# Kernel tuning notes

Measured on AMD Instinct MI355X. Metric: run time of the kernel, lower is better.

## Reference

```python
import jax, jax.numpy as jnp
import numpy as np

B, S, D, H, IT, V = 2, 1024, 1024, 8, 28, 50257
DH = D // H
EPS = jnp.float32(1.1920929e-07)  # torch RMSNorm default eps = finfo(float32).eps


def _rmsnorm(x, w):
    # torch nn.RMSNorm: x * rsqrt(mean(x^2) + eps) * weight
    ms = jnp.mean(jnp.square(x), axis=-1, keepdims=True)
    return x * jax.lax.rsqrt(ms + EPS) * w


def setup_inputs() -> dict:
    key = jax.random.key(0)
    ks = jax.random.split(key, 8)
    s = 0.02
    tokens = jax.random.randint(ks[0], (B, S), 0, V)
    embed = jax.random.normal(ks[1], (V, D), dtype=jnp.float32) * s
    Wk = jax.random.normal(ks[2], (D, D), dtype=jnp.float32) * s
    Wv = jax.random.normal(ks[3], (D, D), dtype=jnp.float32) * s
    Ws = jax.random.normal(ks[4], (D, D), dtype=jnp.float32) * s
    Wo = jax.random.normal(ks[5], (D, D), dtype=jnp.float32) * s  # original zero-inits; randomized for a non-trivial baseline
    step_size = jnp.linspace(0.5, 0.1, IT, dtype=jnp.float32)
    norm_w = jnp.ones((IT, D), jnp.float32)   # per-iteration RMSNorm weight
    gamma = jnp.ones((IT, D), jnp.float32)
    beta = jnp.zeros((IT, D), jnp.float32)
    out_norm_w = jnp.ones((D,), jnp.float32)
    lm_head_w = jax.random.normal(ks[6], (V, D), dtype=jnp.float32) * s
    return dict(tokens=tokens, embed=embed, Wk=Wk, Wv=Wv, Ws=Ws, Wo=Wo,
                step_size=step_size, norm_w=norm_w, gamma=gamma, beta=beta,
                out_norm_w=out_norm_w, lm_head_w=lm_head_w)


def _forward(tokens, embed, Wk, Wv, Ws, Wo, step_size, norm_w, gamma, beta, out_norm_w, lm_head_w):
    b, s = tokens.shape
    causal = jnp.tril(jnp.ones((s, s), dtype=bool))  # allow j <= i
    scale = 1.0 / np.sqrt(DH)

    def compute_force(h):
        k = (h @ Wk.T).reshape(b, s, H, DH)
        v = (h @ Wv.T).reshape(b, s, H, DH)
        energy = jnp.einsum('bihd,bjhd->bhij', k, k) * scale
        logits = jnp.where(causal, -energy, -jnp.inf)  # softmax(-energy) with causal masking
        w = jax.nn.softmax(logits, axis=-1)
        pairwise = jnp.einsum('bhij,bjhd->bihd', w, v).reshape(b, s, D)
        return (pairwise + h @ Ws.T) @ Wo.T

    def step(x, p):
        st, nw, g, bb = p
        h = _rmsnorm(x, nw) * g + bb
        return x + compute_force(h) * st, None

    x0 = embed[tokens].astype(jnp.float32)
    x, _ = jax.lax.scan(jax.checkpoint(step), x0, (step_size, norm_w, gamma, beta))
    x = _rmsnorm(x, out_norm_w)
    return x @ lm_head_w.T  # [B, S, V] logits


def reference(tokens, embed, Wk, Wv, Ws, Wo, step_size, norm_w, gamma, beta, out_norm_w, lm_head_w):
    return _forward(tokens, embed, Wk, Wv, Ws, Wo, step_size, norm_w, gamma, beta, out_norm_w, lm_head_w)
```

## Files before the change

kernel.cpp:

```cpp
#include <hip/hip_runtime.h>
#include <cstdint>
#include <cstddef>

#define S_   1024
#define D_   1024
#define H_   8
#define DH_  128
#define IT_  28
#define V_   50257
#define B_   2
#define ROWS 2048
#define EPS_ 1.1920929e-07f

typedef unsigned short u16;
typedef __attribute__((ext_vector_type(8))) short s8v;
typedef __attribute__((ext_vector_type(4))) float f4v;

static __device__ __forceinline__ void gload16(const void* g, void* l) {
  __builtin_amdgcn_global_load_lds((__attribute__((address_space(1))) void*)(g),
                                   (__attribute__((address_space(3))) void*)(l), 16, 0, 0);
}

static __device__ __forceinline__ u16 f2bf(float f) {
  union { float f; uint32_t u; } v; v.f = f;
  return (u16)((v.u + 0x7FFFu + ((v.u >> 16) & 1u)) >> 16);
}

static __device__ __forceinline__ float wave_sum(float v) {
#pragma unroll
  for (int o = 32; o > 0; o >>= 1) v += __shfl_xor(v, o, 64);
  return v;
}

__device__ __constant__ int IT_TAB[40] = {
  15,15,15,15, 14,14,14, 13,13,13, 12,12,12, 11,11,11,
  10,10, 9,9, 8,8, 7,7, 6, 5, 4, 3,
  14,10,6,2, 13,9,5,1, 12,8,4,0};
__device__ __constant__ int CH_TAB[40] = {
  0,1,2,3, 0,1,2, 0,1,2, 0,1,2, 0,1,2,
  0,1, 0,1, 0,1, 0,1, 0, 0, 0, 0,
  3,2,1,0, 3,2,1,0, 3,2,1,0};

__global__ __launch_bounds__(256) void k_embed(const int* __restrict__ tok,
                                               const float* __restrict__ emb,
                                               float* __restrict__ x) {
  const int row = blockIdx.x;
  const int t = tok[row];
  ((float4*)(x + (size_t)row * D_))[threadIdx.x] =
      ((const float4*)(emb + (size_t)t * D_))[threadIdx.x];
}

__global__ __launch_bounds__(256) void k_cvt(const float* __restrict__ w,
                                             u16* __restrict__ o, int n4) {
  const int idx = blockIdx.x * 256 + threadIdx.x;
  if (idx < n4) {
    const float4 f = ((const float4*)w)[idx];
    ushort4 u;
    u.x = f2bf(f.x); u.y = f2bf(f.y); u.z = f2bf(f.z); u.w = f2bf(f.w);
    ((ushort4*)o)[idx] = u;
  }
}

__global__ __launch_bounds__(256) void k_rmsnorm(const float* __restrict__ x,
                                                 const float* __restrict__ nw,
                                                 const float* __restrict__ g,
                                                 const float* __restrict__ bb,
                                                 u16* __restrict__ h) {
  const int row = blockIdx.x;
  const int tid = threadIdx.x;
  const float4 xv = ((const float4*)(x + (size_t)row * D_))[tid];
  float ss = xv.x*xv.x + xv.y*xv.y + xv.z*xv.z + xv.w*xv.w;
  ss = wave_sum(ss);
  __shared__ float red[4];
  const int lane = tid & 63, wid = tid >> 6;
  if (lane == 0) red[wid] = ss;
  __syncthreads();
  const float tot = red[0] + red[1] + red[2] + red[3];
  const float r = rsqrtf(tot * (1.0f / (float)D_) + EPS_);
  const float4 wv = ((const float4*)nw)[tid];
  float o[4];
  o[0] = xv.x * r * wv.x; o[1] = xv.y * r * wv.y;
  o[2] = xv.z * r * wv.z; o[3] = xv.w * r * wv.w;
  if (g) {
    const float4 gv = ((const float4*)g)[tid];
    const float4 bv = ((const float4*)bb)[tid];
    o[0] = o[0]*gv.x + bv.x; o[1] = o[1]*gv.y + bv.y;
    o[2] = o[2]*gv.z + bv.z; o[3] = o[3]*gv.w + bv.w;
  }
  ushort4 u;
  u.x = f2bf(o[0]); u.y = f2bf(o[1]); u.z = f2bf(o[2]); u.w = f2bf(o[3]);
  ((ushort4*)(h + (size_t)row * D_))[tid] = u;
}

template<int EPI, int SWAP, int NB>
__global__ __launch_bounds__(256) void k_gemm(const u16* __restrict__ A, int lda,
                                              const u16* __restrict__ Bm, int ldb,
                                              float* __restrict__ C, int ldc,
                                              int N, int K,
                                              const float* __restrict__ alphap, int aidx) {
  __shared__ u16 As[128 * 32];
  __shared__ u16 Bs[64 * NB * 32];
  int bid = blockIdx.x + gridDim.x * blockIdx.y;
  if (SWAP) {
    const int nwg = gridDim.x * gridDim.y;
    const int q = nwg >> 3, r = nwg & 7;
    const int xcd = bid & 7, lo = bid >> 3;
    bid = (xcd < r ? xcd * (q + 1) : r * (q + 1) + (xcd - r) * q) + lo;
  }
  const int bx = bid % gridDim.x;
  const int by = bid / gridDim.x;
  const int i0 = (SWAP ? bx : by) * 128;
  const int j0 = (SWAP ? by : bx) * (64 * NB);
  const int tid = threadIdx.x;
  const int lane = tid & 63, w = tid >> 6;
  const int wr = w >> 1, wc = w & 1;
  const int l15 = lane & 15, l4 = lane >> 4;
  const int ar = tid >> 2, ak = (tid & 3) << 3;
  int bj0 = j0 + ar;      if (bj0 > N - 1) bj0 = N - 1;
  int bj1 = j0 + ar + 64; if (bj1 > N - 1) bj1 = N - 1;

  f4v acc[4][2 * NB];
#pragma unroll
  for (int m = 0; m < 4; ++m)
#pragma unroll
    for (int n = 0; n < 2 * NB; ++n) acc[m][n] = (f4v)0.0f;

  for (int k0 = 0; k0 < K; k0 += 32) {
    gload16(A + (size_t)(i0 + ar) * lda + k0 + ak, &As[(size_t)tid * 8]);
    gload16(A + (size_t)(i0 + ar + 64) * lda + k0 + ak, &As[((size_t)tid + 256) * 8]);
    gload16(Bm + (size_t)bj0 * ldb + k0 + ak, &Bs[(size_t)tid * 8]);
    if (NB == 2)
      gload16(Bm + (size_t)bj1 * ldb + k0 + ak, &Bs[((size_t)tid + 256) * 8]);
    __syncthreads();
    s8v a[4], b[2 * NB];
#pragma unroll
    for (int m = 0; m < 4; ++m)
      a[m] = *(const s8v*)&As[(wr * 64 + m * 16 + l15) * 32 + l4 * 8];
#pragma unroll
    for (int n = 0; n < 2 * NB; ++n)
      b[n] = *(const s8v*)&Bs[(wc * 32 * NB + n * 16 + l15) * 32 + l4 * 8];
#pragma unroll
    for (int m = 0; m < 4; ++m)
#pragma unroll
      for (int n = 0; n < 2 * NB; ++n)
        acc[m][n] = __builtin_amdgcn_mfma_f32_16x16x32_bf16(a[m], b[n], acc[m][n], 0, 0, 0);
    __syncthreads();
  }

  const float alpha = alphap ? alphap[aidx] : 1.0f;
#pragma unroll
  for (int m = 0; m < 4; ++m) {
#pragma unroll
    for (int n = 0; n < 2 * NB; ++n) {
      const int i = i0 + wr * 64 + m * 16 + l4 * 4;
      const int j = j0 + wc * 32 * NB + n * 16 + l15;
      const f4v v = acc[m][n];
      if (EPI == 0) {
        if (j < N) {
#pragma unroll
          for (int r = 0; r < 4; ++r) C[(size_t)(i + r) * ldc + j] = v[r];
        }
      } else {
#pragma unroll
        for (int r = 0; r < 4; ++r) C[(size_t)(i + r) * ldc + j] += alpha * v[r];
      }
    }
  }
}

__global__ __launch_bounds__(256) void k_gemm_qkv(const u16* __restrict__ A,
                                                  const u16* __restrict__ Wcat,
                                                  u16* __restrict__ kb,
                                                  u16* __restrict__ vt,
                                                  float* __restrict__ fb) {
  __shared__ u16 As[128 * 32];
  __shared__ u16 Bs[64 * 32];
  const int i0 = blockIdx.y * 128, j0 = blockIdx.x * 64;
  const int tid = threadIdx.x;
  const int lane = tid & 63, w = tid >> 6;
  const int wr = w >> 1, wc = w & 1;
  const int l15 = lane & 15, l4 = lane >> 4;
  const int ar = tid >> 2, ak = (tid & 3) << 3;

  f4v acc[4][2];
#pragma unroll
  for (int m = 0; m < 4; ++m)
#pragma unroll
    for (int n = 0; n < 2; ++n) acc[m][n] = (f4v)0.0f;

  for (int k0 = 0; k0 < D_; k0 += 32) {
    gload16(A + (size_t)(i0 + ar) * D_ + k0 + ak, &As[(size_t)tid * 8]);
    gload16(A + (size_t)(i0 + ar + 64) * D_ + k0 + ak, &As[((size_t)tid + 256) * 8]);
    gload16(Wcat + (size_t)(j0 + ar) * D_ + k0 + ak, &Bs[(size_t)tid * 8]);
    __syncthreads();
    s8v a[4], b[2];
#pragma unroll
    for (int m = 0; m < 4; ++m)
      a[m] = *(const s8v*)&As[(wr * 64 + m * 16 + l15) * 32 + l4 * 8];
#pragma unroll
    for (int n = 0; n < 2; ++n)
      b[n] = *(const s8v*)&Bs[(wc * 32 + n * 16 + l15) * 32 + l4 * 8];
#pragma unroll
    for (int m = 0; m < 4; ++m)
#pragma unroll
      for (int n = 0; n < 2; ++n)
        acc[m][n] = __builtin_amdgcn_mfma_f32_16x16x32_bf16(a[m], b[n], acc[m][n], 0, 0, 0);
    __syncthreads();
  }

#pragma unroll
  for (int m = 0; m < 4; ++m) {
#pragma unroll
    for (int n = 0; n < 2; ++n) {
      const int i = i0 + wr * 64 + m * 16 + l4 * 4;
      const int j = j0 + wc * 32 + n * 16 + l15;
      const int sel = j >> 10, jl = j & 1023;
      const f4v v = acc[m][n];
      if (sel == 0) {
#pragma unroll
        for (int r = 0; r < 4; ++r) kb[(size_t)(i + r) * D_ + jl] = f2bf(v[r]);
      } else if (sel == 1) {
        ushort4 p;
        p.x = f2bf(v[0]); p.y = f2bf(v[1]); p.z = f2bf(v[2]); p.w = f2bf(v[3]);
        *(ushort4*)&vt[((size_t)(i >> 10) * D_ + jl) * S_ + (i & 1023)] = p;
      } else {
#pragma unroll
        for (int r = 0; r < 4; ++r) fb[(size_t)(i + r) * D_ + jl] = v[r];
      }
    }
  }
}

__global__ __launch_bounds__(256) void k_attn_part(const u16* __restrict__ kb,
                                                   const u16* __restrict__ vt,
                                                   float* __restrict__ po,
                                                   float* __restrict__ pml,
                                                   float scale) {
  const int it = IT_TAB[blockIdx.x], ch = CH_TAB[blockIdx.x];
  const int z = blockIdx.y;
  const int b = z >> 3, h = z & 7;
  const u16* Kbh = kb + (size_t)b * S_ * D_ + h * DH_;
  const u16* Vth = vt + ((size_t)b * D_ + h * DH_) * S_;
  const int i0 = it * 64;
  const int jt0 = ch * 4;
  const int jtend = min(jt0 + 4, it + 1);
  __shared__ u16 Kj[64 * 128];
  __shared__ u16 Vj[128 * 64];
  __shared__ u16 Pl[4][16 * 64];
  const int tid = threadIdx.x;
  const int lane = tid & 63, w = tid >> 6;
  const int l15 = lane & 15, l4 = lane >> 4;

  s8v ka[4];
#pragma unroll
  for (int ks = 0; ks < 4; ++ks)
    ka[ks] = *(const s8v*)(Kbh + (size_t)(i0 + w * 16 + l15) * D_ + ks * 32 + l4 * 8);

  f4v acc_o[8];
#pragma unroll
  for (int n = 0; n < 8; ++n) acc_o[n] = (f4v)0.0f;
  float mrow[4], lrow[4];
#pragma unroll
  for (int r = 0; r < 4; ++r) { mrow[r] = -3.0e38f; lrow[r] = 0.f; }

  const int krow = tid >> 4, koff = (tid & 15) * 8;
  const int vrow = tid >> 3, voff = (tid & 7) * 8;

  for (int jt = jt0; jt < jtend; ++jt) {
    const int j0 = jt * 64;
#pragma unroll
    for (int p = 0; p < 4; ++p) {
      const int row = p * 16 + krow;
      gload16(Kbh + (size_t)(j0 + row) * D_ + (koff ^ ((row & 7) << 3)),
              &Kj[(size_t)(p * 256 + tid) * 8]);
    }
#pragma unroll
    for (int p = 0; p < 4; ++p) {
      const int row = p * 32 + vrow;
      gload16(Vth + (size_t)row * S_ + j0 + (voff ^ ((row & 7) << 3)),
              &Vj[(size_t)(p * 256 + tid) * 8]);
    }
    __syncthreads();

    f4v s[4];
#pragma unroll
    for (int n = 0; n < 4; ++n) s[n] = (f4v)0.0f;
#pragma unroll
    for (int ks = 0; ks < 4; ++ks) {
#pragma unroll
      for (int n = 0; n < 4; ++n) {
        const int row = n * 16 + l15;
        const s8v kf = *(const s8v*)&Kj[row * 128 + ((ks * 32 + l4 * 8) ^ ((row & 7) << 3))];
        s[n] = __builtin_amdgcn_mfma_f32_16x16x32_bf16(ka[ks], kf, s[n], 0, 0, 0);
      }
    }

    float pv[4][4], tmax[4];
#pragma unroll
    for (int r = 0; r < 4; ++r) tmax[r] = -3.0e38f;
#pragma unroll
    for (int n = 0; n < 4; ++n) {
      const int j = j0 + n * 16 + l15;
#pragma unroll
      for (int r = 0; r < 4; ++r) {
        const int i = i0 + w * 16 + l4 * 4 + r;
        const float lg = (j <= i) ? (-scale * s[n][r]) : -3.0e38f;
        pv[n][r] = lg;
        tmax[r] = fmaxf(tmax[r], lg);
      }
    }
#pragma unroll
    for (int r = 0; r < 4; ++r) {
#pragma unroll
      for (int o = 8; o > 0; o >>= 1) tmax[r] = fmaxf(tmax[r], __shfl_xor(tmax[r], o, 64));
    }
    float es[4];
#pragma unroll
    for (int r = 0; r < 4; ++r) {
      const float mn = fmaxf(mrow[r], tmax[r]);
      es[r] = __expf(mrow[r] - mn);
      mrow[r] = mn;
    }
    float psum[4] = {0.f, 0.f, 0.f, 0.f};
#pragma unroll
    for (int n = 0; n < 4; ++n) {
#pragma unroll
      for (int r = 0; r < 4; ++r) {
        const float p = __expf(pv[n][r] - mrow[r]);
        pv[n][r] = p;
        psum[r] += p;
      }
    }
#pragma unroll
    for (int r = 0; r < 4; ++r) {
#pragma unroll
      for (int o = 8; o > 0; o >>= 1) psum[r] += __shfl_xor(psum[r], o, 64);
      lrow[r] = lrow[r] * es[r] + psum[r];
    }
#pragma unroll
    for (int n = 0; n < 8; ++n) {
      f4v t = acc_o[n];
      t[0] *= es[0]; t[1] *= es[1]; t[2] *= es[2]; t[3] *= es[3];
      acc_o[n] = t;
    }

    u16* P = Pl[w];
#pragma unroll
    for (int n = 0; n < 4; ++n) {
#pragma unroll
      for (int r = 0; r < 4; ++r) {
        const int row = l4 * 4 + r;
        P[row * 64 + ((n * 16 + l15) ^ ((row & 7) << 3))] = f2bf(pv[n][r]);
      }
    }
    __syncthreads();
    s8v pa[2];
#pragma unroll
    for (int kp = 0; kp < 2; ++kp)
      pa[kp] = *(const s8v*)&P[l15 * 64 + ((kp * 32 + l4 * 8) ^ ((l15 & 7) << 3))];

#pragma unroll
    for (int kp = 0; kp < 2; ++kp) {
#pragma unroll
      for (int n = 0; n < 8; ++n) {
        const int d = n * 16 + l15;
        const s8v vf = *(const s8v*)&Vj[d * 64 + ((kp * 32 + l4 * 8) ^ ((d & 7) << 3))];
        acc_o[n] = __builtin_amdgcn_mfma_f32_16x16x32_bf16(pa[kp], vf, acc_o[n], 0, 0, 0);
      }
    }
    __syncthreads();
  }

  const int slot = (z * 16 + it) * 4 + ch;
  float* O = po + (size_t)slot * (64 * 128);
#pragma unroll
  for (int n = 0; n < 8; ++n) {
#pragma unroll
    for (int r = 0; r < 4; ++r)
      O[(w * 16 + l4 * 4 + r) * 128 + n * 16 + l15] = acc_o[n][r];
  }
  if (l15 == 0) {
#pragma unroll
    for (int r = 0; r < 4; ++r) {
      const int row = w * 16 + l4 * 4 + r;
      pml[(size_t)slot * 128 + row] = mrow[r];
      pml[(size_t)slot * 128 + 64 + row] = lrow[r];
    }
  }
}

__global__ __launch_bounds__(256) void k_attn_merge(const float* __restrict__ po,
                                                    const float* __restrict__ pml,
                                                    const float* __restrict__ fb,
                                                    u16* __restrict__ fbh) {
  const int it = blockIdx.x, z = blockIdx.y;
  const int b = z >> 3, h = z & 7;
  const int nch = (it >> 2) + 1;
  const int row = threadIdx.x >> 2;
  const int cseg = (threadIdx.x & 3) * 32;
  const int base = (z * 16 + it) * 4;

  float ms = -3.0e38f, mv[4], lv[4];
#pragma unroll
  for (int c = 0; c < 4; ++c)
    if (c < nch) {
      mv[c] = pml[(size_t)(base + c) * 128 + row];
      lv[c] = pml[(size_t)(base + c) * 128 + 64 + row];
      ms = fmaxf(ms, mv[c]);
    }
  float ls = 0.f, fac[4];
#pragma unroll
  for (int c = 0; c < 4; ++c)
    if (c < nch) { fac[c] = __expf(mv[c] - ms); ls += lv[c] * fac[c]; }
  const float inv = 1.0f / ls;

  float4 o[8];
#pragma unroll
  for (int q = 0; q < 8; ++q) o[q] = make_float4(0.f, 0.f, 0.f, 0.f);
#pragma unroll
  for (int c = 0; c < 4; ++c)
    if (c < nch) {
      const float4* Oc = (const float4*)(po + (size_t)(base + c) * (64 * 128) + row * 128 + cseg);
      const float f = fac[c];
#pragma unroll
      for (int q = 0; q < 8; ++q) {
        const float4 t = Oc[q];
        o[q].x += t.x * f; o[q].y += t.y * f; o[q].z += t.z * f; o[q].w += t.w * f;
      }
    }

  const size_t gidx = ((size_t)(b * S_ + it * 64 + row)) * D_ + h * DH_ + cseg;
  const float4* F = (const float4*)(fb + gidx);
  u16* out = fbh + gidx;
#pragma unroll
  for (int q = 0; q < 8; ++q) {
    const float4 fv = F[q];
    ushort4 u;
    u.x = f2bf(fv.x + o[q].x * inv);
    u.y = f2bf(fv.y + o[q].y * inv);
    u.z = f2bf(fv.z + o[q].z * inv);
    u.w = f2bf(fv.w + o[q].w * inv);
    *(ushort4*)(out + q * 4) = u;
  }
}

extern "C" void kernel_launch(void* const* d_in, const int* in_sizes, int n_in,
                              void* d_out, int out_size, void* d_ws, size_t ws_size,
                              hipStream_t stream) {
  const int*   tok = (const int*)  d_in[0];
  const float* emb = (const float*)d_in[1];
  const float* Wk  = (const float*)d_in[2];
  const float* Wv  = (const float*)d_in[3];
  const float* Ws  = (const float*)d_in[4];
  const float* Wo  = (const float*)d_in[5];
  const float* stp = (const float*)d_in[6];
  const float* nw  = (const float*)d_in[7];
  const float* gam = (const float*)d_in[8];
  const float* bet = (const float*)d_in[9];
  const float* onw = (const float*)d_in[10];
  const float* lmw = (const float*)d_in[11];
  float* out = (float*)d_out;

  uint8_t* wsb = (uint8_t*)d_ws;
  float* x   = (float*)wsb;  wsb += (size_t)ROWS * D_ * 4;
  u16* hb    = (u16*)wsb;    wsb += (size_t)ROWS * D_ * 2;
  u16* kb    = (u16*)wsb;    wsb += (size_t)ROWS * D_ * 2;
  u16* vt    = (u16*)wsb;    wsb += (size_t)ROWS * D_ * 2;
  float* fb  = (float*)wsb;  wsb += (size_t)ROWS * D_ * 4;
  u16* fbh   = (u16*)wsb;    wsb += (size_t)ROWS * D_ * 2;
  u16* Wcat  = (u16*)wsb;    wsb += (size_t)3 * D_ * D_ * 2;
  u16* Wob   = (u16*)wsb;    wsb += (size_t)D_ * D_ * 2;
  float* po  = (float*)wsb;  wsb += (size_t)1024 * 64 * 128 * 4;
  float* pml = (float*)wsb;  wsb += (size_t)1024 * 128 * 4;
  u16* Wlm   = (u16*)wsb;    wsb += (size_t)V_ * D_ * 2;

  const float scale = 0.08838834764831845f;
  const int n4 = D_ * D_ / 4;

  k_cvt<<<1024, 256, 0, stream>>>(Wk, Wcat, n4);
  k_cvt<<<1024, 256, 0, stream>>>(Wv, Wcat + (size_t)D_ * D_, n4);
  k_cvt<<<1024, 256, 0, stream>>>(Ws, Wcat + (size_t)2 * D_ * D_, n4);
  k_cvt<<<1024, 256, 0, stream>>>(Wo, Wob, n4);
  k_embed<<<ROWS, 256, 0, stream>>>(tok, emb, x);

  for (int it = 0; it < IT_; ++it) {
    k_rmsnorm<<<ROWS, 256, 0, stream>>>(x, nw + (size_t)it * D_,
                                        gam + (size_t)it * D_, bet + (size_t)it * D_, hb);
    k_gemm_qkv<<<dim3(48, 16), 256, 0, stream>>>(hb, Wcat, kb, vt, fb);
    k_attn_part<<<dim3(40, 16), 256, 0, stream>>>(kb, vt, po, pml, scale);
    k_attn_merge<<<dim3(16, 16), 256, 0, stream>>>(po, pml, fb, fbh);
    k_gemm<1, 0, 1><<<dim3(16, 16), 256, 0, stream>>>(fbh, D_, Wob, D_, x, D_, D_, D_, stp, it);
  }

  k_rmsnorm<<<ROWS, 256, 0, stream>>>(x, onw, nullptr, nullptr, hb);

  k_cvt<<<(V_ * 256 + 255) / 256, 256, 0, stream>>>(lmw, Wlm, V_ * D_ / 4);
  k_gemm<0, 1, 2><<<dim3(16, (V_ + 127) / 128), 256, 0, stream>>>(hb, D_, Wlm, D_, out, V_, V_, D_,
                                                                  nullptr, 0);
}
```

Baseline: 2.914 ms.

## Double-buffer LDS tiles in GEMM kernels to overlap global loads with MFMA

```diff
diff --git a/kernel.cpp b/kernel.cpp
--- a/kernel.cpp
+++ b/kernel.cpp
@@ -15,6 +15,10 @@
 typedef unsigned short u16;
 typedef __attribute__((ext_vector_type(8))) short s8v;
 typedef __attribute__((ext_vector_type(4))) float f4v;
+
+#define VMCNT0 asm volatile("s_waitcnt vmcnt(0)" ::: "memory")
+#define LGKM0  asm volatile("s_waitcnt lgkmcnt(0)" ::: "memory")
+#define RBAR   do { __builtin_amdgcn_s_barrier(); asm volatile("" ::: "memory"); } while (0)
 
 static __device__ __forceinline__ void gload16(const void* g, void* l) {
   __builtin_amdgcn_global_load_lds((__attribute__((address_space(1))) void*)(g),
@@ -98,19 +102,10 @@
                                               float* __restrict__ C, int ldc,
                                               int N, int K,
                                               const float* __restrict__ alphap, int aidx) {
-  __shared__ u16 As[128 * 32];
-  __shared__ u16 Bs[64 * NB * 32];
-  int bid = blockIdx.x + gridDim.x * blockIdx.y;
-  if (SWAP) {
-    const int nwg = gridDim.x * gridDim.y;
-    const int q = nwg >> 3, r = nwg & 7;
-    const int xcd = bid & 7, lo = bid >> 3;
-    bid = (xcd < r ? xcd * (q + 1) : r * (q + 1) + (xcd - r) * q) + lo;
-  }
-  const int bx = bid % gridDim.x;
-  const int by = bid / gridDim.x;
-  const int i0 = (SWAP ? bx : by) * 128;
-  const int j0 = (SWAP ? by : bx) * (64 * NB);
+  __shared__ u16 As0[128 * 32], As1[128 * 32];
+  __shared__ u16 Bs0[64 * NB * 32], Bs1[64 * NB * 32];
+  const int i0 = (SWAP ? blockIdx.x : blockIdx.y) * 128;
+  const int j0 = (SWAP ? blockIdx.y : blockIdx.x) * (64 * NB);
   const int tid = threadIdx.x;
   const int lane = tid & 63, w = tid >> 6;
   const int wr = w >> 1, wc = w & 1;
@@ -125,26 +120,42 @@
 #pragma unroll
     for (int n = 0; n < 2 * NB; ++n) acc[m][n] = (f4v)0.0f;
 
-  for (int k0 = 0; k0 < K; k0 += 32) {
-    gload16(A + (size_t)(i0 + ar) * lda + k0 + ak, &As[(size_t)tid * 8]);
-    gload16(A + (size_t)(i0 + ar + 64) * lda + k0 + ak, &As[((size_t)tid + 256) * 8]);
-    gload16(Bm + (size_t)bj0 * ldb + k0 + ak, &Bs[(size_t)tid * 8]);
+  auto STAGE = [&](u16* AsB, u16* BsB, int k0) {
+    gload16(A + (size_t)(i0 + ar) * lda + k0 + ak, AsB + (size_t)tid * 8);
+    gload16(A + (size_t)(i0 + ar + 64) * lda + k0 + ak, AsB + ((size_t)tid + 256) * 8);
+    gload16(Bm + (size_t)bj0 * ldb + k0 + ak, BsB + (size_t)tid * 8);
     if (NB == 2)
-      gload16(Bm + (size_t)bj1 * ldb + k0 + ak, &Bs[((size_t)tid + 256) * 8]);
-    __syncthreads();
+      gload16(Bm + (size_t)bj1 * ldb + k0 + ak, BsB + ((size_t)tid + 256) * 8);
+  };
+  auto COMP = [&](const u16* AsB, const u16* BsB) {
     s8v a[4], b[2 * NB];
 #pragma unroll
     for (int m = 0; m < 4; ++m)
-      a[m] = *(const s8v*)&As[(wr * 64 + m * 16 + l15) * 32 + l4 * 8];
+      a[m] = *(const s8v*)&AsB[(wr * 64 + m * 16 + l15) * 32 + l4 * 8];
 #pragma unroll
     for (int n = 0; n < 2 * NB; ++n)
-      b[n] = *(const s8v*)&Bs[(wc * 32 * NB + n * 16 + l15) * 32 + l4 * 8];
+      b[n] = *(const s8v*)&BsB[(wc * 32 * NB + n * 16 + l15) * 32 + l4 * 8];
+    LGKM0;
 #pragma unroll
     for (int m = 0; m < 4; ++m)
 #pragma unroll
       for (int n = 0; n < 2 * NB; ++n)
         acc[m][n] = __builtin_amdgcn_mfma_f32_16x16x32_bf16(a[m], b[n], acc[m][n], 0, 0, 0);
-    __syncthreads();
+  };
+
+  STAGE(As0, Bs0, 0);
+  VMCNT0;
+  RBAR;
+
+  for (int k0 = 0; k0 < K; k0 += 64) {
+    STAGE(As1, Bs1, k0 + 32);
+    COMP(As0, Bs0);
+    VMCNT0;
+    RBAR;
+    if (k0 + 64 < K) STAGE(As0, Bs0, k0 + 64);
+    COMP(As1, Bs1);
+    VMCNT0;
+    RBAR;
   }
 
   const float alpha = alphap ? alphap[aidx] : 1.0f;
@@ -173,8 +184,8 @@
                                                   u16* __restrict__ kb,
                                                   u16* __restrict__ vt,
                                                   float* __restrict__ fb) {
-  __shared__ u16 As[128 * 32];
-  __shared__ u16 Bs[64 * 32];
+  __shared__ u16 As0[128 * 32], As1[128 * 32];
+  __shared__ u16 Bs0[64 * 32], Bs1[64 * 32];
   const int i0 = blockIdx.y * 128, j0 = blockIdx.x * 64;
   const int tid = threadIdx.x;
   const int lane = tid & 63, w = tid >> 6;
@@ -188,24 +199,39 @@
 #pragma unroll
     for (int n = 0; n < 2; ++n) acc[m][n] = (f4v)0.0f;
 
-  for (int k0 = 0; k0 < D_; k0 += 32) {
-    gload16(A + (size_t)(i0 + ar) * D_ + k0 + ak, &As[(size_t)tid * 8]);
-    gload16(A + (size_t)(i0 + ar + 64) * D_ + k0 + ak, &As[((size_t)tid + 256) * 8]);
-    gload16(Wcat + (size_t)(j0 + ar) * D_ + k0 + ak, &Bs[(size_t)tid * 8]);
-    __syncthreads();
+  auto STAGE = [&](u16* AsB, u16* BsB, int k0) {
+    gload16(A + (size_t)(i0 + ar) * D_ + k0 + ak, AsB + (size_t)tid * 8);
+    gload16(A + (size_t)(i0 + ar + 64) * D_ + k0 + ak, AsB + ((size_t)tid + 256) * 8);
+    gload16(Wcat + (size_t)(j0 + ar) * D_ + k0 + ak, BsB + (size_t)tid * 8);
+  };
+  auto COMP = [&](const u16* AsB, const u16* BsB) {
     s8v a[4], b[2];
 #pragma unroll
     for (int m = 0; m < 4; ++m)
-      a[m] = *(const s8v*)&As[(wr * 64 + m * 16 + l15) * 32 + l4 * 8];
+      a[m] = *(const s8v*)&AsB[(wr * 64 + m * 16 + l15) * 32 + l4 * 8];
 #pragma unroll
     for (int n = 0; n < 2; ++n)
-      b[n] = *(const s8v*)&Bs[(wc * 32 + n * 16 + l15) * 32 + l4 * 8];
+      b[n] = *(const s8v*)&BsB[(wc * 32 + n * 16 + l15) * 32 + l4 * 8];
+    LGKM0;
 #pragma unroll
     for (int m = 0; m < 4; ++m)
 #pragma unroll
       for (int n = 0; n < 2; ++n)
         acc[m][n] = __builtin_amdgcn_mfma_f32_16x16x32_bf16(a[m], b[n], acc[m][n], 0, 0, 0);
-    __syncthreads();
+  };
+
+  STAGE(As0, Bs0, 0);
+  VMCNT0;
+  RBAR;
+  for (int k0 = 0; k0 < D_; k0 += 64) {
+    STAGE(As1, Bs1, k0 + 32);
+    COMP(As0, Bs0);
+    VMCNT0;
+    RBAR;
+    if (k0 + 64 < D_) STAGE(As0, Bs0, k0 + 64);
+    COMP(As1, Bs1);
+    VMCNT0;
+    RBAR;
   }
 
 #pragma unroll
```

Result: no change. 2.861 ms (-1.8%).
